# Kernel tuning notes

Measured on AMD Instinct MI355X. Metric: run time of the kernel, lower is better.

The kernel has to match this reference:

```python
import jax, jax.numpy as jnp
import numpy as np

BATCH, IN_SIZE, CH, DIM, MODES, LAYERS, PROJ, OUT = 16, 1, 128, 128, 32, 4, 128, 1


def setup_inputs() -> dict:
    key = jax.random.key(0)
    ks = jax.random.split(key, 12)
    scale = 1.0 / (CH * CH)
    inp = {
        "z": jax.random.normal(ks[0], (BATCH, IN_SIZE, DIM, DIM), dtype=jnp.float32),
        # Lifting: pointwise linear input_size -> channels
        "lift_w": jax.random.normal(ks[1], (CH, IN_SIZE), dtype=jnp.float32) / np.sqrt(IN_SIZE),
        "lift_b": jnp.zeros((CH,), dtype=jnp.float32),
        # Spectral conv weights per layer, two mode corners, complex stored as real/imag
        "wr1": scale * jax.random.normal(ks[2], (LAYERS, CH, CH, MODES, MODES), dtype=jnp.float32),
        "wi1": scale * jax.random.normal(ks[3], (LAYERS, CH, CH, MODES, MODES), dtype=jnp.float32),
        "wr2": scale * jax.random.normal(ks[4], (LAYERS, CH, CH, MODES, MODES), dtype=jnp.float32),
        "wi2": scale * jax.random.normal(ks[5], (LAYERS, CH, CH, MODES, MODES), dtype=jnp.float32),
        # Projection: channels -> projection_size -> output_size (pointwise MLP)
        "pw1": jax.random.normal(ks[6], (PROJ, CH), dtype=jnp.float32) / np.sqrt(CH),
        "pb1": jnp.zeros((PROJ,), dtype=jnp.float32),
        "pw2": jax.random.normal(ks[7], (OUT, PROJ), dtype=jnp.float32) / np.sqrt(PROJ),
        "pb2": jnp.zeros((OUT,), dtype=jnp.float32),
    }
    return inp


def _spectral_conv(v, w1, w2, modes, size):
    # v: [b, c, X, Y] real; rfft2 over last two dims (norm='backward')
    vf = jnp.fft.rfft2(v, norm="backward")  # [b, c, X, Y//2+1] complex
    of = jnp.zeros_like(vf)
    # low-frequency corner
    of = of.at[:, :, :modes, :modes].set(
        jnp.einsum("bixy,ioxy->boxy", vf[:, :, :modes, :modes], w1))
    # high (negative) frequency corner along first spatial axis
    of = of.at[:, :, -modes:, :modes].set(
        jnp.einsum("bixy,ioxy->boxy", vf[:, :, -modes:, :modes], w2))
    return jnp.fft.irfft2(of, s=(size, size), norm="backward")


def reference(z, lift_w, lift_b, wr1, wi1, wr2, wi2, pw1, pb1, pw2, pb2):
    n_layers = wr1.shape[0]
    modes = wr1.shape[-1]
    size = z.shape[-1]
    # Lifting: [b, in, x, y] -> [b, ch, x, y]
    v = jnp.einsum("bixy,ci->bcxy", z, lift_w) + lift_b[None, :, None, None]
    out = v
    for l in range(n_layers):
        w1 = wr1[l] + 1j * wi1[l]
        w2 = wr2[l] + 1j * wi2[l]
        out = _spectral_conv(out, w1, w2, modes, size)
    # Projection MLP (pointwise over grid)
    h = jnp.einsum("bcxy,pc->bpxy", out, pw1) + pb1[None, :, None, None]
    h = jax.nn.gelu(h)
    out = jnp.einsum("bpxy,op->boxy", h, pw2) + pb2[None, :, None, None]
    return out
```

## Files before the change

### kernel.cpp

```cpp
#include <hip/hip_runtime.h>
#include <math.h>

#define B 16
#define CH 128
#define DIM 128
#define MODES 32
#define NLAYERS 4
#define PROJ 128
#define U 64
#define KY 32
#define NMODE (U*KY)
#define N2 (DIM*DIM)
#define PG 16
#define PPG (PROJ/PG)

__device__ __forceinline__ void async16(const void* g, void* l) {
  __builtin_amdgcn_global_load_lds((const __attribute__((address_space(1))) unsigned int*)g,
                                   (__attribute__((address_space(3))) unsigned int*)l, 16, 0, 0);
}

__global__ __launch_bounds__(256) void k_zf1(const float* __restrict__ z,
                                             float2* __restrict__ t1) {
  __shared__ float zrow[16][DIM];
  __shared__ float2 tw[DIM];
  int bid = blockIdx.x;
  int b = bid >> 3, xt = bid & 7;
  int x0 = xt * 16;
  int t = threadIdx.x;
  if (t < 128) {
    float ang = (float)(2.0 * M_PI) * (float)t / 128.0f;
    tw[t] = make_float2(cosf(ang), sinf(ang));
  }
  for (int e = t; e < 16 * DIM / 4; e += 256)
    ((float4*)&zrow[0][0])[e] = ((const float4*)&z[b * N2 + x0 * DIM])[e];
  __syncthreads();
  #pragma unroll
  for (int j = 0; j < 2; ++j) {
    int it = t + j * 256;
    int x_l = it >> 5, ky = it & 31;
    float tr = 0.f, ti = 0.f;
    int tt = 0;
    for (int y = 0; y < DIM; ++y) {
      float v = zrow[x_l][y];
      float2 w = tw[tt];
      tr += v * w.x;
      ti -= v * w.y;
      tt = (tt + ky) & 127;
    }
    t1[((size_t)b * DIM + x0 + x_l) * KY + ky] = make_float2(tr, ti);
  }
}

__global__ __launch_bounds__(256) void k_zf2(const float2* __restrict__ t1,
                                             float* __restrict__ zfr, float* __restrict__ zfi) {
  __shared__ float2 t1s[DIM][KY];
  __shared__ float2 tw[DIM];
  int bid = blockIdx.x;
  int b = bid >> 1, uh = bid & 1;
  int t = threadIdx.x;
  if (t < 128) {
    float ang = (float)(2.0 * M_PI) * (float)t / 128.0f;
    tw[t] = make_float2(cosf(ang), sinf(ang));
  }
  for (int e = t; e < DIM * KY / 2; e += 256)
    ((float4*)&t1s[0][0])[e] = ((const float4*)&t1[(size_t)b * DIM * KY])[e];
  __syncthreads();
  #pragma unroll
  for (int j = 0; j < 4; ++j) {
    int m = t + j * 256;
    int u_l = m >> 5, ky = m & 31;
    int u = uh * 32 + u_l;
    int kx = (u < 32) ? u : (u + 64);
    float ar = 0.f, ai = 0.f;
    int tt = 0;
    for (int x = 0; x < DIM; ++x) {
      float2 v = t1s[x][ky];
      float2 w = tw[tt];
      ar += v.x * w.x + v.y * w.y;
      ai += v.y * w.x - v.x * w.y;
      tt = (tt + kx) & 127;
    }
    zfr[b * NMODE + u * KY + ky] = ar;
    zfi[b * NMODE + u * KY + ky] = ai;
  }
}

__global__ __launch_bounds__(256) void k_lift(const float* __restrict__ zfr, const float* __restrict__ zfi,
                                              const float* __restrict__ lw, const float* __restrict__ lb,
                                              float2* __restrict__ vcout) {
  int idx = blockIdx.x * 256 + threadIdx.x;
  if (idx >= B * CH * NMODE) return;
  int m = idx & (NMODE - 1);
  int c = (idx >> 11) & 127;
  int b = idx >> 18;
  float w = lw[c];
  float re = w * zfr[b * NMODE + m];
  float im = w * zfi[b * NMODE + m];
  if (m == 0) re += 16384.f * lb[c];
  vcout[idx] = make_float2(re, im);
}

__global__ __launch_bounds__(256) void k_spec(const float2* __restrict__ vc,
                                              const float* __restrict__ wr1, const float* __restrict__ wi1,
                                              const float* __restrict__ wr2, const float* __restrict__ wi2,
                                              float2* __restrict__ oc) {
  __shared__ float lW[2][2][4][16][32];
  __shared__ float2 lV[2][4][16][32];
  int bid = blockIdx.x;
  int u = ((bid & 7) << 3) | ((bid >> 3) & 7);
  int ot = bid >> 6;
  int o0 = ot * 16;
  int kxw = u & 31;
  const float* wr = (u >= 32) ? wr2 : wr1;
  const float* wi = (u >= 32) ? wi2 : wi1;
  int t = threadIdx.x;
  int ky = t & 31, oq = t >> 5;
  int wv = t >> 6, lane = t & 63;
  float accR[2][16] = {}, accI[2][16] = {};

  #define STAGE(bf, i0)                                                              \
    {                                                                                \
      if (wv < 2) {                                                                  \
        _Pragma("unroll")                                                            \
        for (int n = 0; n < 8; ++n) {                                                \
          int nu = wv * 8 + n;                                                       \
          int ri = nu >> 3, il = (nu >> 1) & 3;                                      \
          int o_l = (nu & 1) * 8 + (lane >> 3), ky4 = (lane & 7) * 4;                \
          const float* src = (ri ? wi : wr) +                                        \
            (((size_t)((i0) + il) * CH + o0 + o_l) * MODES + kxw) * MODES + ky4;     \
          async16(src, (char*)&lW[bf][0][0][0][0] + (size_t)nu * 1024 + lane * 16);  \
        }                                                                            \
      } else {                                                                       \
        _Pragma("unroll")                                                            \
        for (int n = 0; n < 8; ++n) {                                                \
          int nu = (wv - 2) * 8 + n;                                                 \
          int il = nu >> 2;                                                          \
          int b_l = (nu & 3) * 4 + (lane >> 4), ky2 = (lane & 15) * 2;               \
          const float2* src = vc + ((size_t)b_l * CH + (i0) + il) * NMODE +          \
                              u * KY + ky2;                                          \
          async16(src, (char*)&lV[bf][0][0][0] + (size_t)nu * 1024 + lane * 16);     \
        }                                                                            \
      }                                                                              \
    }

  STAGE(0, 0);
  for (int k = 0; k < 32; ++k) {
    int cur = k & 1;
    __syncthreads();
    if (k + 1 < 32) STAGE(cur ^ 1, (k + 1) * 4);
    #pragma unroll
    for (int il = 0; il < 4; ++il) {
      float wrv[2], wiv[2];
      #pragma unroll
      for (int j = 0; j < 2; ++j) {
        wrv[j] = lW[cur][0][il][oq * 2 + j][ky];
        wiv[j] = lW[cur][1][il][oq * 2 + j][ky];
      }
      #pragma unroll
      for (int bb = 0; bb < 16; ++bb) {
        float2 v = lV[cur][il][bb][ky];
        #pragma unroll
        for (int j = 0; j < 2; ++j) {
          accR[j][bb] += wrv[j] * v.x - wiv[j] * v.y;
          accI[j][bb] += wrv[j] * v.y + wiv[j] * v.x;
        }
      }
    }
  }
  #undef STAGE
  #pragma unroll
  for (int j = 0; j < 2; ++j)
    #pragma unroll
    for (int bb = 0; bb < 16; ++bb) {
      int o = o0 + oq * 2 + j;
      oc[(((size_t)bb * CH + o) * U + u) * KY + ky] = make_float2(accR[j][bb], accI[j][bb]);
    }
}

__global__ __launch_bounds__(256) void k_proj0(float2* __restrict__ vc) {
  int idx = blockIdx.x * 256 + threadIdx.x;
  if (idx >= B * CH * 33) return;
  int pi = idx % 33;
  int bc = idx / 33;
  float2* base = vc + (size_t)bc * NMODE;
  if (pi == 0) {
    base[0].y = 0.f;
  } else if (pi == 32) {
    base[32 * KY].x *= 0.5f;
    base[32 * KY].y *= 0.5f;
  } else {
    int ua = pi, ub = 64 - pi;
    float2 a = base[ua * KY], b2 = base[ub * KY];
    base[ua * KY] = make_float2(0.5f * (a.x + b2.x), 0.5f * (a.y - b2.y));
    base[ub * KY] = make_float2(0.5f * (b2.x + a.x), 0.5f * (b2.y - a.y));
  }
}

__global__ __launch_bounds__(256) void k_pw1(const float2* __restrict__ xc,
                                             const float* __restrict__ pw1,
                                             float2* __restrict__ hc) {
  __shared__ float wT[CH][CH + 1];
  int bid = blockIdx.x;
  int b = bid >> 5, jt = bid & 31;
  int t = threadIdx.x;
  for (int e = t; e < CH * CH; e += 256) {
    int p = e >> 7, c = e & 127;
    wT[c][p] = pw1[e];
  }
  __syncthreads();
  int tx = t & 15, ty = t >> 4;
  int j0 = jt * 64 + tx * 4;
  float accR[4][8] = {}, accI[4][8] = {};
  for (int c = 0; c < CH; ++c) {
    const float4* x4 = (const float4*)&xc[((size_t)b * CH + c) * NMODE + j0];
    float4 v0 = x4[0], v1 = x4[1];
    float xrv[4] = {v0.x, v0.z, v1.x, v1.z};
    float xiv[4] = {v0.y, v0.w, v1.y, v1.w};
    float w[8];
    #pragma unroll
    for (int pp = 0; pp < 8; ++pp) w[pp] = wT[c][ty * 8 + pp];
    #pragma unroll
    for (int jj = 0; jj < 4; ++jj)
      #pragma unroll
      for (int pp = 0; pp < 8; ++pp) {
        accR[jj][pp] += w[pp] * xrv[jj];
        accI[jj][pp] += w[pp] * xiv[jj];
      }
  }
  #pragma unroll
  for (int pp = 0; pp < 8; ++pp) {
    int p = ty * 8 + pp;
    float4* o4 = (float4*)&hc[((size_t)b * CH + p) * NMODE + j0];
    o4[0] = make_float4(accR[0][pp], accI[0][pp], accR[1][pp], accI[1][pp]);
    o4[1] = make_float4(accR[2][pp], accI[2][pp], accR[3][pp], accI[3][pp]);
  }
}

__global__ __launch_bounds__(256) void k_idft_partial(const float2* __restrict__ hc,
                                                      const float* __restrict__ pb1,
                                                      const float* __restrict__ pw2,
                                                      float* __restrict__ partial) {
  __shared__ float2 tw[DIM];
  __shared__ float2 hfs[2][NMODE];
  __shared__ float2 sbuf[16][KY];
  int bid = blockIdx.x;
  int b = (bid & 7) | (((bid >> 3) & 1) << 3);
  int pg = (bid >> 4) & 15, xs = bid >> 8;
  int x0 = xs * 8;
  int t = threadIdx.x;
  int wv = t >> 6, lane = t & 63;
  if (t < 128) {
    float ang = (float)(2.0 * M_PI) * (float)t / 128.0f;
    tw[t] = make_float2(cosf(ang), sinf(ang));
  }

  #define STAGE_H(bf, pp_)                                                           \
    {                                                                                \
      const char* srcb = (const char*)(hc + ((size_t)b * CH + pg * PPG + (pp_)) * NMODE); \
      _Pragma("unroll")                                                              \
      for (int n = 0; n < 4; ++n) {                                                  \
        int nu = wv * 4 + n;                                                         \
        async16(srcb + (size_t)nu * 1024 + lane * 16,                                \
                (char*)&hfs[bf][0] + (size_t)nu * 1024 + lane * 16);                 \
      }                                                                              \
    }

  STAGE_H(0, 0);
  __syncthreads();
  int y = t & 63, xh = t >> 6;
  float Cr[KY], Sr[KY];
  #pragma unroll
  for (int ky = 0; ky < KY; ++ky) {
    float2 w = tw[(ky * y) & 127];
    float wk = (ky == 0) ? 1.f : 2.f;
    Cr[ky] = wk * w.x;
    Sr[ky] = -wk * w.y;
  }
  int xqA = t >> 5, kyA = t & 31;
  int xA = x0 + xqA;
  float res[8] = {0.f, 0.f, 0.f, 0.f, 0.f, 0.f, 0.f, 0.f};
  for (int pp = 0; pp < PPG; ++pp) {
    int p = pg * PPG + pp;
    int cur = pp & 1;
    if (pp) __syncthreads();
    if (pp + 1 < PPG) STAGE_H(cur ^ 1, pp + 1);
    {
      float per = 0.f, pei = 0.f, por = 0.f, poi = 0.f;
      int tt = 0;
      #pragma unroll
      for (int uu = 0; uu < 32; uu += 2) {
        float2 w0 = tw[tt];
        float2 h0 = hfs[cur][uu * KY + kyA];
        per += h0.x * w0.x - h0.y * w0.y;
        pei += h0.x * w0.y + h0.y * w0.x;
        tt = (tt + xA) & 127;
        float2 w1 = tw[tt];
        float2 h1 = hfs[cur][(uu + 1) * KY + kyA];
        por += h1.x * w1.x - h1.y * w1.y;
        poi += h1.x * w1.y + h1.y * w1.x;
        tt = (tt + xA) & 127;
      }
      tt = (96 * xA) & 127;
      #pragma unroll
      for (int uu = 32; uu < 64; uu += 2) {
        float2 w0 = tw[tt];
        float2 h0 = hfs[cur][uu * KY + kyA];
        per += h0.x * w0.x - h0.y * w0.y;
        pei += h0.x * w0.y + h0.y * w0.x;
        tt = (tt + xA) & 127;
        float2 w1 = tw[tt];
        float2 h1 = hfs[cur][(uu + 1) * KY + kyA];
        por += h1.x * w1.x - h1.y * w1.y;
        poi += h1.x * w1.y + h1.y * w1.x;
        tt = (tt + xA) & 127;
      }
      sbuf[xqA][kyA]     = make_float2(per + por, pei + poi);
      sbuf[xqA + 8][kyA] = make_float2(per - por, pei - poi);
    }
    __syncthreads();
    float pb = pb1[p], pw = pw2[p];
    #pragma unroll
    for (int sl = 0; sl < 4; ++sl) {
      int s_i = xh + sl * 4;
      float ae = 0.f, ao = 0.f;
      #pragma unroll
      for (int ky = 0; ky < KY; ky += 2) {
        float4 v = *(const float4*)&sbuf[s_i][ky];
        ae += v.x * Cr[ky] + v.y * Sr[ky];
        ao += v.z * Cr[ky + 1] + v.w * Sr[ky + 1];
      }
      float hlo = (ae + ao) * (1.f / 16384.f) + pb;
      float hhi = (ae - ao) * (1.f / 16384.f) + pb;
      float zlo = 1.5957691216057308f * (hlo + 0.044715f * hlo * hlo * hlo);
      float zhi = 1.5957691216057308f * (hhi + 0.044715f * hhi * hhi * hhi);
      res[sl * 2]     += pw * (hlo / (1.f + __expf(-zlo)));
      res[sl * 2 + 1] += pw * (hhi / (1.f + __expf(-zhi)));
    }
  }
  #undef STAGE_H
  size_t pbase = ((size_t)pg * B + b) * N2;
  #pragma unroll
  for (int sl = 0; sl < 4; ++sl) {
    int s_i = xh + sl * 4;
    int x = x0 + (s_i & 7) + ((s_i >> 3) << 6);
    partial[pbase + x * DIM + y]      = res[sl * 2];
    partial[pbase + x * DIM + y + 64] = res[sl * 2 + 1];
  }
}

__global__ __launch_bounds__(256) void k_reduce(const float* __restrict__ partial,
                                                const float* __restrict__ pb2,
                                                float* __restrict__ outp) {
  int idx = blockIdx.x * 256 + threadIdx.x;
  if (idx >= B * N2) return;
  float s = pb2[0];
  #pragma unroll
  for (int pg = 0; pg < PG; ++pg) s += partial[(size_t)pg * B * N2 + idx];
  outp[idx] = s;
}

extern "C" void kernel_launch(void* const* d_in, const int* in_sizes, int n_in,
                              void* d_out, int out_size, void* d_ws, size_t ws_size,
                              hipStream_t stream) {
  const float* z   = (const float*)d_in[0];
  const float* lw  = (const float*)d_in[1];
  const float* lb  = (const float*)d_in[2];
  const float* wr1 = (const float*)d_in[3];
  const float* wi1 = (const float*)d_in[4];
  const float* wr2 = (const float*)d_in[5];
  const float* wi2 = (const float*)d_in[6];
  const float* pw1 = (const float*)d_in[7];
  const float* pb1 = (const float*)d_in[8];
  const float* pw2 = (const float*)d_in[9];
  const float* pb2 = (const float*)d_in[10];
  float* out = (float*)d_out;
  float* ws = (float*)d_ws;

  float* zfr = ws;
  float* zfi = zfr + 32768;
  float2* Ac = (float2*)(ws + 65536);
  float2* Bc = Ac + (size_t)B * CH * NMODE;
  float2* t1 = Bc;

  k_zf1<<<B * 8, 256, 0, stream>>>(z, t1);
  k_zf2<<<B * 2, 256, 0, stream>>>(t1, zfr, zfi);
  k_lift<<<(B * CH * NMODE) / 256, 256, 0, stream>>>(zfr, zfi, lw, lb, Ac);

  const size_t WSTRIDE = (size_t)CH * CH * MODES * MODES;
  float2 *ir = Ac, *oc = Bc;
  for (int l = 0; l < NLAYERS; ++l) {
    k_spec<<<512, 256, 0, stream>>>(ir,
                                    wr1 + l * WSTRIDE, wi1 + l * WSTRIDE,
                                    wr2 + l * WSTRIDE, wi2 + l * WSTRIDE,
                                    oc);
    if (l < NLAYERS - 1)
      k_proj0<<<(B * CH * 33 + 255) / 256, 256, 0, stream>>>(oc);
    float2* tmp = ir; ir = oc; oc = tmp;
  }
  k_pw1<<<512, 256, 0, stream>>>(ir, pw1, oc);
  float* partial = (float*)ir;
  k_idft_partial<<<B * PG * 8, 256, 0, stream>>>(oc, pb1, pw2, partial);
  k_reduce<<<(B * N2) / 256, 256, 0, stream>>>(partial, pb2, out);
}
```

Baseline: 814.2 us.

## Retile spectral mixing, double projection groups, use direct twiddle indexing and fast reciprocal

Several independent changes. The spectral-mixing kernel now has each thread compute 4 output channels by 8 batches instead of 2 by 16, which changes the balance of shared-memory reads against FMAs. Twiddle indices in the DFT loops are computed directly from the loop index instead of a running accumulator, so unrolled iterations no longer depend on each other. The projection kernel doubles its group count (PG 32), giving more blocks with fewer channels each, and its GELU divide becomes a hardware reciprocal. One pointwise-channel kernel also remaps block indices across batches, and the larger PG means more partial-sum buffer traffic in the final reduction.

```diff
diff --git a/kernel.cpp b/kernel.cpp
--- a/kernel.cpp
+++ b/kernel.cpp
@@ -11,7 +11,7 @@
 #define KY 32
 #define NMODE (U*KY)
 #define N2 (DIM*DIM)
-#define PG 16
+#define PG 32
 #define PPG (PROJ/PG)
 
 __device__ __forceinline__ void async16(const void* g, void* l) {
@@ -39,13 +39,11 @@
     int it = t + j * 256;
     int x_l = it >> 5, ky = it & 31;
     float tr = 0.f, ti = 0.f;
-    int tt = 0;
     for (int y = 0; y < DIM; ++y) {
       float v = zrow[x_l][y];
-      float2 w = tw[tt];
+      float2 w = tw[(ky * y) & 127];
       tr += v * w.x;
       ti -= v * w.y;
-      tt = (tt + ky) & 127;
     }
     t1[((size_t)b * DIM + x0 + x_l) * KY + ky] = make_float2(tr, ti);
   }
@@ -72,13 +70,11 @@
     int u = uh * 32 + u_l;
     int kx = (u < 32) ? u : (u + 64);
     float ar = 0.f, ai = 0.f;
-    int tt = 0;
     for (int x = 0; x < DIM; ++x) {
       float2 v = t1s[x][ky];
-      float2 w = tw[tt];
+      float2 w = tw[(kx * x) & 127];
       ar += v.x * w.x + v.y * w.y;
       ai += v.y * w.x - v.x * w.y;
-      tt = (tt + kx) & 127;
     }
     zfr[b * NMODE + u * KY + ky] = ar;
     zfi[b * NMODE + u * KY + ky] = ai;
@@ -114,9 +110,9 @@
   const float* wr = (u >= 32) ? wr2 : wr1;
   const float* wi = (u >= 32) ? wi2 : wi1;
   int t = threadIdx.x;
-  int ky = t & 31, oq = t >> 5;
+  int ky = t & 31, bh = (t >> 5) & 1, oq = t >> 6;
   int wv = t >> 6, lane = t & 63;
-  float accR[2][16] = {}, accI[2][16] = {};
+  float accR[4][8] = {}, accI[4][8] = {};
 
   #define STAGE(bf, i0)                                                              \
     {                                                                                \
@@ -150,17 +146,17 @@
     if (k + 1 < 32) STAGE(cur ^ 1, (k + 1) * 4);
     #pragma unroll
     for (int il = 0; il < 4; ++il) {
-      float wrv[2], wiv[2];
-      #pragma unroll
-      for (int j = 0; j < 2; ++j) {
-        wrv[j] = lW[cur][0][il][oq * 2 + j][ky];
-        wiv[j] = lW[cur][1][il][oq * 2 + j][ky];
-      }
-      #pragma unroll
-      for (int bb = 0; bb < 16; ++bb) {
-        float2 v = lV[cur][il][bb][ky];
+      float wrv[4], wiv[4];
+      #pragma unroll
+      for (int j = 0; j < 4; ++j) {
+        wrv[j] = lW[cur][0][il][oq * 4 + j][ky];
+        wiv[j] = lW[cur][1][il][oq * 4 + j][ky];
+      }
+      #pragma unroll
+      for (int bb = 0; bb < 8; ++bb) {
+        float2 v = lV[cur][il][bh * 8 + bb][ky];
         #pragma unroll
-        for (int j = 0; j < 2; ++j) {
+        for (int j = 0; j < 4; ++j) {
           accR[j][bb] += wrv[j] * v.x - wiv[j] * v.y;
           accI[j][bb] += wrv[j] * v.y + wiv[j] * v.x;
         }
@@ -169,11 +165,11 @@
   }
   #undef STAGE
   #pragma unroll
-  for (int j = 0; j < 2; ++j)
-    #pragma unroll
-    for (int bb = 0; bb < 16; ++bb) {
-      int o = o0 + oq * 2 + j;
-      oc[(((size_t)bb * CH + o) * U + u) * KY + ky] = make_float2(accR[j][bb], accI[j][bb]);
+  for (int j = 0; j < 4; ++j)
+    #pragma unroll
+    for (int bb = 0; bb < 8; ++bb) {
+      int o = o0 + oq * 4 + j, b = bh * 8 + bb;
+      oc[(((size_t)b * CH + o) * U + u) * KY + ky] = make_float2(accR[j][bb], accI[j][bb]);
     }
 }
 
@@ -201,7 +197,8 @@
                                              float2* __restrict__ hc) {
   __shared__ float wT[CH][CH + 1];
   int bid = blockIdx.x;
-  int b = bid >> 5, jt = bid & 31;
+  int b = ((bid & 7) << 1) | ((bid >> 8) & 1);
+  int jt = (bid >> 3) & 31;
   int t = threadIdx.x;
   for (int e = t; e < CH * CH; e += 256) {
     int p = e >> 7, c = e & 127;
@@ -245,7 +242,7 @@
   __shared__ float2 sbuf[16][KY];
   int bid = blockIdx.x;
   int b = (bid & 7) | (((bid >> 3) & 1) << 3);
-  int pg = (bid >> 4) & 15, xs = bid >> 8;
+  int pg = (bid >> 4) & 31, xs = bid >> 9;
   int x0 = xs * 8;
   int t = threadIdx.x;
   int wv = t >> 6, lane = t & 63;
@@ -286,33 +283,27 @@
     if (pp + 1 < PPG) STAGE_H(cur ^ 1, pp + 1);
     {
       float per = 0.f, pei = 0.f, por = 0.f, poi = 0.f;
-      int tt = 0;
       #pragma unroll
       for (int uu = 0; uu < 32; uu += 2) {
-        float2 w0 = tw[tt];
+        float2 w0 = tw[(uu * xA) & 127];
         float2 h0 = hfs[cur][uu * KY + kyA];
         per += h0.x * w0.x - h0.y * w0.y;
         pei += h0.x * w0.y + h0.y * w0.x;
-        tt = (tt + xA) & 127;
-        float2 w1 = tw[tt];
+        float2 w1 = tw[((uu + 1) * xA) & 127];
         float2 h1 = hfs[cur][(uu + 1) * KY + kyA];
         por += h1.x * w1.x - h1.y * w1.y;
         poi += h1.x * w1.y + h1.y * w1.x;
-        tt = (tt + xA) & 127;
-      }
-      tt = (96 * xA) & 127;
+      }
       #pragma unroll
       for (int uu = 32; uu < 64; uu += 2) {
-        float2 w0 = tw[tt];
+        float2 w0 = tw[((uu + 64) * xA) & 127];
         float2 h0 = hfs[cur][uu * KY + kyA];
         per += h0.x * w0.x - h0.y * w0.y;
         pei += h0.x * w0.y + h0.y * w0.x;
-        tt = (tt + xA) & 127;
-        float2 w1 = tw[tt];
+        float2 w1 = tw[((uu + 65) * xA) & 127];
         float2 h1 = hfs[cur][(uu + 1) * KY + kyA];
         por += h1.x * w1.x - h1.y * w1.y;
         poi += h1.x * w1.y + h1.y * w1.x;
-        tt = (tt + xA) & 127;
       }
       sbuf[xqA][kyA]     = make_float2(per + por, pei + poi);
       sbuf[xqA + 8][kyA] = make_float2(per - por, pei - poi);
@@ -333,8 +324,8 @@
       float hhi = (ae - ao) * (1.f / 16384.f) + pb;
       float zlo = 1.5957691216057308f * (hlo + 0.044715f * hlo * hlo * hlo);
       float zhi = 1.5957691216057308f * (hhi + 0.044715f * hhi * hhi * hhi);
-      res[sl * 2]     += pw * (hlo / (1.f + __expf(-zlo)));
-      res[sl * 2 + 1] += pw * (hhi / (1.f + __expf(-zhi)));
+      res[sl * 2]     += pw * hlo * __builtin_amdgcn_rcpf(1.f + __expf(-zlo));
+      res[sl * 2 + 1] += pw * hhi * __builtin_amdgcn_rcpf(1.f + __expf(-zhi));
     }
   }
   #undef STAGE_H
```

Result: faster. 793.0 us (-2.6%).
